# Kernel optimization log

Hardware: AMD Instinct MI355X
Metric: run time of the kernel (lower is better)

Reference implementation:

```python
import jax, jax.numpy as jnp
import numpy as np

B, S, D, H = 2, 2048, 1024, 16
DK = D // H


def setup_inputs() -> dict:
    key = jax.random.key(0)
    ks = jax.random.split(key, 9)
    s = 1.0 / np.sqrt(D)
    return {
        "x": jax.random.normal(ks[0], (B, S, D), dtype=jnp.float32),
        "wq": jax.random.normal(ks[1], (D, D), dtype=jnp.float32) * s,
        "bq": jax.random.normal(ks[2], (D,), dtype=jnp.float32) * 0.01,
        "wk": jax.random.normal(ks[3], (D, D), dtype=jnp.float32) * s,
        "bk": jax.random.normal(ks[4], (D,), dtype=jnp.float32) * 0.01,
        "wv": jax.random.normal(ks[5], (D, D), dtype=jnp.float32) * s,
        "bv": jax.random.normal(ks[6], (D,), dtype=jnp.float32) * 0.01,
        "wo": jax.random.normal(ks[7], (D, D), dtype=jnp.float32) * s,
        "bo": jax.random.normal(ks[8], (D,), dtype=jnp.float32) * 0.01,
    }


def reference(x, wq, bq, wk, bk, wv, bv, wo, bo):
    b, s, d = x.shape
    # Linear layers use torch convention: y = x @ W.T + b
    def proj(w, bias):
        y = jnp.einsum("bsd,ed->bse", x, w) + bias
        return y.reshape(b, s, H, DK).transpose(0, 2, 1, 3)  # (B,H,S,DK)

    q = proj(wq, bq)
    k = proj(wk, bk)
    v = proj(wv, bv)

    # Because each Q-chunk attends to the full K/V with m initialized to -inf,
    # the chunked online-softmax loop is exactly full softmax attention.
    scores = jnp.einsum("bhqd,bhkd->bhqk", q, k) / jnp.sqrt(jnp.float32(DK))
    attn = jax.nn.softmax(scores, axis=-1)
    out = jnp.einsum("bhqk,bhkd->bhqd", attn, v)  # (B,H,S,DK)

    out = out.transpose(0, 2, 1, 3).reshape(b, s, d)
    return jnp.einsum("bsd,ed->bse", out, wo) + bo
```

## Files before the change

kernel.cpp:

```cpp
#include <hip/hip_runtime.h>

typedef __attribute__((ext_vector_type(8))) short s16x8;
typedef __attribute__((ext_vector_type(4))) short s16x4;
typedef __attribute__((ext_vector_type(4))) float f32x4;

#define DEVI static __device__ __forceinline__

DEVI short f2bf(float f) {
  union { float f; unsigned u; } v; v.f = f;
  unsigned u = v.u;
  unsigned r = u + 0x7FFFu + ((u >> 16) & 1u);
  return (short)(r >> 16);
}
DEVI short f2bf_fast(float f) {
  union { float f; unsigned u; } v; v.f = f;
  return (short)((v.u + 0x8000u) >> 16);
}
DEVI float bf2f(short s) {
  union { unsigned u; float f; } v;
  v.u = ((unsigned)(unsigned short)s) << 16;
  return v.f;
}
DEVI f32x4 mfma16(s16x8 a, s16x8 b, f32x4 c) {
  return __builtin_amdgcn_mfma_f32_16x16x32_bf16(a, b, c, 0, 0, 0);
}
DEVI float fexp2(float x) {
#if __has_builtin(__builtin_amdgcn_exp2f)
  return __builtin_amdgcn_exp2f(x);
#else
  float r; asm("v_exp_f32 %0, %1" : "=v"(r) : "v"(x)); return r;
#endif
}
DEVI void gld16(const void* g, void* l) {
  __builtin_amdgcn_global_load_lds(
      (const __attribute__((address_space(1))) void*)g,
      (__attribute__((address_space(3))) void*)l, 16, 0, 0);
}

constexpr int Sc = 2048, Dc = 1024, Hc = 16, DKc = 64;
constexpr int Mc = 4096;

__global__ void detect_ker(const unsigned short* __restrict__ x, int* __restrict__ flag) {
  __shared__ int cnt;
  if (threadIdx.x == 0) cnt = 0;
  __syncthreads();
  int c = 0;
  for (int i = threadIdx.x; i < 4096; i += 256) {
    int e = (x[i] >> 7) & 0xFF;
    if (e >= 140) c++;
  }
  atomicAdd(&cnt, c);
  __syncthreads();
  if (threadIdx.x == 0) *flag = (cnt > 64) ? 1 : 0;
}

__global__ void norm_all(const void* x,
                         const void* w0, const void* w1, const void* w2, const void* w3,
                         const void* b0, const void* b1, const void* b2, const void* b3,
                         short* __restrict__ xdst, short* __restrict__ wdst,
                         float* __restrict__ bdst, const int* __restrict__ flag) {
  const int f = *flag;
  const int blk = blockIdx.x, tid = threadIdx.x;
  if (blk < 8192) {
    const void* src; short* dst; int i;
    if (blk < 4096) {
      i = blk * 256 + tid; src = x; dst = xdst;
    } else {
      int j = (blk - 4096) * 256 + tid;
      int region = j >> 18;
      const void* ws[4] = {w0, w1, w2, w3};
      src = ws[region]; dst = wdst + (size_t)region * 1048576;
      i = j & 262143;
    }
    if (f) {
      f32x4 v = ((const f32x4*)src)[i];
      s16x4 o;
#pragma unroll
      for (int j2 = 0; j2 < 4; ++j2) o[j2] = f2bf(v[j2]);
      ((s16x4*)dst)[i] = o;
    } else {
      ((s16x4*)dst)[i] = ((const s16x4*)src)[i];
    }
  } else {
    const void* bs[4] = {b0, b1, b2, b3};
#pragma unroll
    for (int j = 0; j < 16; ++j) {
      int i = tid + j * 256;
      int r = i >> 10, k = i & 1023;
      bdst[i] = f ? ((const float*)bs[r])[k] : bf2f(((const short*)bs[r])[k]);
    }
  }
}

template <int EPI>
__global__ __launch_bounds__(256, 2)
void gemm_bt(const short* __restrict__ A, const short* __restrict__ Wbase,
             const float* __restrict__ bias_c, short* __restrict__ outQKV,
             short* __restrict__ outV, void* __restrict__ outFinal,
             const int* __restrict__ flag) {
  constexpr int K = Dc, N = Dc;
  const int z = blockIdx.z;
  const short* W = Wbase + (size_t)z * N * K;
  const float* bias = bias_c + (size_t)z * N;
  const float oscale = (EPI == 0 && z == 0) ? 0.125f * 1.44269504f : 1.0f;

  __shared__ short lA[128 * 64];
  __shared__ short lB[128 * 64];

  const int tid = threadIdx.x;
  const int lane = tid & 63, wave = tid >> 6;
  const int l16 = lane & 15, quad = lane >> 4;
  const int wm0 = (wave >> 1) * 64, wn0 = (wave & 1) * 64;
  const int m0 = blockIdx.y * 128, n0 = blockIdx.x * 128;
  const int lr = lane >> 3;
  const int cg = ((lane & 7) ^ lr) * 8;
  const int x7 = l16 & 7;

  f32x4 acc[4][4] = {};

  for (int k0 = 0; k0 < K; k0 += 64) {
    __syncthreads();
#pragma unroll
    for (int it = 0; it < 4; ++it) {
      int rbase = wave * 32 + it * 8;
      gld16(&A[(size_t)(m0 + rbase + lr) * K + k0 + cg], &lA[rbase * 64]);
      gld16(&W[(size_t)(n0 + rbase + lr) * K + k0 + cg], &lB[rbase * 64]);
    }
    __syncthreads();
#pragma unroll
    for (int ks = 0; ks < 2; ++ks) {
      const int sw = ((ks * 4 + quad) ^ x7) * 8;
      s16x8 af[4], bfr[4];
#pragma unroll
      for (int i = 0; i < 4; ++i) {
        af[i]  = *(const s16x8*)&lA[(wm0 + i * 16 + l16) * 64 + sw];
        bfr[i] = *(const s16x8*)&lB[(wn0 + i * 16 + l16) * 64 + sw];
      }
#pragma unroll
      for (int mi = 0; mi < 4; ++mi)
#pragma unroll
        for (int ni = 0; ni < 4; ++ni)
          acc[mi][ni] = mfma16(af[mi], bfr[ni], acc[mi][ni]);
    }
  }

  if constexpr (EPI == 0) {
    if (z == 2) {
#pragma unroll
      for (int ni = 0; ni < 4; ++ni) {
        int n = n0 + wn0 + ni * 16 + l16;
        float bv = bias[n];
        int h = (n >> 6) & 15, dk = n & 63;
#pragma unroll
        for (int mi = 0; mi < 4; ++mi) {
          int mbase = m0 + wm0 + mi * 16 + quad * 4;
          int bb = mbase >> 11, s = mbase & 2047;
          s16x4 pk;
#pragma unroll
          for (int r = 0; r < 4; ++r) pk[r] = f2bf(acc[mi][ni][r] + bv);
          *(s16x4*)&outV[(((size_t)(bb * Hc + h)) * DKc + dk) * Sc + s] = pk;
        }
      }
      return;
    }
#pragma unroll
    for (int ni = 0; ni < 4; ++ni) {
      int n = n0 + wn0 + ni * 16 + l16;
      float bv = bias[n];
#pragma unroll
      for (int mi = 0; mi < 4; ++mi) {
#pragma unroll
        for (int r = 0; r < 4; ++r) {
          int m = m0 + wm0 + mi * 16 + quad * 4 + r;
          float v = (acc[mi][ni][r] + bv) * oscale;
          int bb = m >> 11, s = m & 2047, h = n >> 6, dk = n & 63;
          size_t idx = ((((size_t)bb * Hc + h) * Sc) + s) * DKc + dk +
                       (size_t)z * Mc * N;
          outQKV[idx] = f2bf(v);
        }
      }
    }
  } else {
    int f32out = *flag;
#pragma unroll
    for (int ni = 0; ni < 4; ++ni) {
      int n = n0 + wn0 + ni * 16 + l16;
      float bv = bias[n];
#pragma unroll
      for (int mi = 0; mi < 4; ++mi) {
#pragma unroll
        for (int r = 0; r < 4; ++r) {
          int m = m0 + wm0 + mi * 16 + quad * 4 + r;
          float v = acc[mi][ni][r] + bv;
          if (f32out) ((float*)outFinal)[(size_t)m * N + n] = v;
          else        ((short*)outFinal)[(size_t)m * N + n] = f2bf(v);
        }
      }
    }
  }
}

__global__ __launch_bounds__(256, 2)
void attn_ker(const short* __restrict__ Q, const short* __restrict__ Kg,
              const short* __restrict__ Vt, short* __restrict__ O) {
  __shared__ short lK[2][64 * 64];
  __shared__ short lV[2][64 * 64];
  __shared__ short lP[4][32][72];

  const int tid = threadIdx.x;
  const int lane = tid & 63, wave = tid >> 6;
  const int l16 = lane & 15, quad = lane >> 4;
  const int lr = lane >> 3;
  const int cg = ((lane & 7) ^ lr) * 8;
  const int x7 = l16 & 7;

  const int bh = blockIdx.y;
  const short* Qb = Q + (size_t)bh * Sc * DKc;
  const short* Kb = Kg + (size_t)bh * Sc * DKc;
  const short* Vb = Vt + (size_t)bh * DKc * Sc;

  const int q0 = blockIdx.x * 128 + wave * 32;

  s16x8 qf[2][2];
#pragma unroll
  for (int mi = 0; mi < 2; ++mi)
#pragma unroll
    for (int ks = 0; ks < 2; ++ks)
      qf[mi][ks] = *(const s16x8*)&Qb[(size_t)(q0 + mi * 16 + l16) * DKc + ks * 32 + quad * 8];

  s16x8 ones = {};
  if (l16 == 0) {
#pragma unroll
    for (int j = 0; j < 8; ++j) ones[j] = (short)0x3F80;
  }
  const f32x4 initC = {-24.f, -24.f, -24.f, -24.f};

  f32x4 oacc[2][4] = {};
  f32x4 oln[2] = {};

#define STAGE(BUF, KB)                                                          \
  {                                                                             \
    _Pragma("unroll")                                                           \
    for (int it = 0; it < 2; ++it) {                                            \
      int rbase = wave * 16 + it * 8;                                           \
      gld16(&Kb[(size_t)((KB) + rbase + lr) * DKc + cg], &lK[BUF][rbase * 64]); \
      gld16(&Vb[(size_t)(rbase + lr) * Sc + (KB) + cg], &lV[BUF][rbase * 64]);  \
    }                                                                           \
  }

  STAGE(0, 0)

  for (int kt = 0; kt < Sc / 64; ++kt) {
    const int p = kt & 1;
    __syncthreads();
    if (kt + 1 < Sc / 64) STAGE(p ^ 1, (kt + 1) * 64)

    f32x4 sacc[2][4];
    {
      const int sw0 = (quad ^ x7) * 8;
      s16x8 kf[4];
#pragma unroll
      for (int ni = 0; ni < 4; ++ni)
        kf[ni] = *(const s16x8*)&lK[p][(ni * 16 + l16) * 64 + sw0];
#pragma unroll
      for (int mi = 0; mi < 2; ++mi)
#pragma unroll
        for (int ni = 0; ni < 4; ++ni)
          sacc[mi][ni] = mfma16(qf[mi][0], kf[ni], initC);
    }
    {
      const int sw1 = ((4 + quad) ^ x7) * 8;
      s16x8 kf[4];
#pragma unroll
      for (int ni = 0; ni < 4; ++ni)
        kf[ni] = *(const s16x8*)&lK[p][(ni * 16 + l16) * 64 + sw1];
#pragma unroll
      for (int mi = 0; mi < 2; ++mi)
#pragma unroll
        for (int ni = 0; ni < 4; ++ni)
          sacc[mi][ni] = mfma16(qf[mi][1], kf[ni], sacc[mi][ni]);
    }

    s16x8 vf[2][4];
#pragma unroll
    for (int ks = 0; ks < 2; ++ks) {
      const int sw = ((ks * 4 + quad) ^ x7) * 8;
#pragma unroll
      for (int ni = 0; ni < 4; ++ni)
        vf[ks][ni] = *(const s16x8*)&lV[p][(ni * 16 + l16) * 64 + sw];
    }

#pragma unroll
    for (int mi = 0; mi < 2; ++mi)
#pragma unroll
      for (int r = 0; r < 4; ++r) {
        int row = mi * 16 + quad * 4 + r;
#pragma unroll
        for (int ni = 0; ni < 4; ++ni)
          lP[wave][row][ni * 16 + l16] = f2bf_fast(fexp2(sacc[mi][ni][r]));
      }

    __builtin_amdgcn_s_waitcnt(0xc07f);

    s16x8 pf[2][2];
#pragma unroll
    for (int mi = 0; mi < 2; ++mi)
#pragma unroll
      for (int ks = 0; ks < 2; ++ks)
        pf[mi][ks] = *(const s16x8*)&lP[wave][mi * 16 + l16][ks * 32 + quad * 8];

#pragma unroll
    for (int ks = 0; ks < 2; ++ks) {
#pragma unroll
      for (int mi = 0; mi < 2; ++mi) {
#pragma unroll
        for (int ni = 0; ni < 4; ++ni)
          oacc[mi][ni] = mfma16(pf[mi][ks], vf[ks][ni], oacc[mi][ni]);
        oln[mi] = mfma16(pf[mi][ks], ones, oln[mi]);
      }
    }
  }
#undef STAGE

  const int bb = bh >> 4, h = bh & 15;
#pragma unroll
  for (int mi = 0; mi < 2; ++mi) {
#pragma unroll
    for (int r = 0; r < 4; ++r) {
      float l = __shfl(oln[mi][r], lane & 48);
      float inv = 1.0f / l;
      int srow = q0 + mi * 16 + quad * 4 + r;
#pragma unroll
      for (int ni = 0; ni < 4; ++ni) {
        int col = h * DKc + ni * 16 + l16;
        O[((size_t)(bb * Sc + srow)) * Dc + col] = f2bf(oacc[mi][ni][r] * inv);
      }
    }
  }
}

extern "C" void kernel_launch(void* const* d_in, const int* in_sizes, int n_in,
                              void* d_out, int out_size, void* d_ws, size_t ws_size,
                              hipStream_t stream) {
  const void* x  = d_in[0];
  const void* wq = d_in[1]; const void* bq = d_in[2];
  const void* wk = d_in[3]; const void* bk = d_in[4];
  const void* wv = d_in[5]; const void* bv = d_in[6];
  const void* wo = d_in[7]; const void* bo = d_in[8];

  char* wsb = (char*)d_ws;
  int*   flag = (int*)wsb;
  short* x_c  = (short*)(wsb + 1024);
  short* w_c  = x_c + (size_t)4 * 1024 * 1024;
  float* b_c  = (float*)(wsb + 1024 + 16 * 1024 * 1024);
  short* Qc   = (short*)(wsb + 1024 + 16 * 1024 * 1024 + 16384);
  short* Kc   = Qc + (size_t)4 * 1024 * 1024;
  short* Vtc  = Kc + (size_t)4 * 1024 * 1024;
  short* Oc   = Vtc + (size_t)4 * 1024 * 1024;

  detect_ker<<<1, 256, 0, stream>>>((const unsigned short*)x, flag);

  norm_all<<<8193, 256, 0, stream>>>(x, wq, wk, wv, wo, bq, bk, bv, bo,
                                     x_c, w_c, b_c, flag);

  gemm_bt<0><<<dim3(8, 32, 3), 256, 0, stream>>>(x_c, w_c, b_c, Qc, Vtc,
                                                 nullptr, flag);

  attn_ker<<<dim3(16, 32), 256, 0, stream>>>(Qc, Kc, Vtc, Oc);

  gemm_bt<1><<<dim3(8, 32, 1), 256, 0, stream>>>(Oc, w_c + 3 * 1048576,
                                                 b_c + 3 * 1024, nullptr, nullptr,
                                                 d_out, flag);
}
```

Measured before the change: 214.4 us.

## Skip bf16 copy pass and split attention into 8 waves of 16 query rows

When the inputs are already bf16, the normalization kernel no longer copies x and the weights into the workspace. The GEMMs read the original buffers directly, picking them by the runtime flag. The attention kernel moves from 4 waves with 32 query rows each to 8 waves with 16 rows each at 512 threads. It also swaps grid axes so blocks sharing a head are adjacent, and computes P before loading V fragments. This cuts copy traffic and per-wave register pressure for more occupancy, at the cost of more K/V LDS reads per query row.

Result: faster. 204.8 us (-4.5%).

```diff
diff --git a/kernel.cpp b/kernel.cpp
--- a/kernel.cpp
+++ b/kernel.cpp
@@ -62,6 +62,7 @@
   const int f = *flag;
   const int blk = blockIdx.x, tid = threadIdx.x;
   if (blk < 8192) {
+    if (!f) return;
     const void* src; short* dst; int i;
     if (blk < 4096) {
       i = blk * 256 + tid; src = x; dst = xdst;
@@ -72,15 +73,11 @@
       src = ws[region]; dst = wdst + (size_t)region * 1048576;
       i = j & 262143;
     }
-    if (f) {
-      f32x4 v = ((const f32x4*)src)[i];
-      s16x4 o;
-#pragma unroll
-      for (int j2 = 0; j2 < 4; ++j2) o[j2] = f2bf(v[j2]);
-      ((s16x4*)dst)[i] = o;
-    } else {
-      ((s16x4*)dst)[i] = ((const s16x4*)src)[i];
-    }
+    f32x4 v = ((const f32x4*)src)[i];
+    s16x4 o;
+#pragma unroll
+    for (int j2 = 0; j2 < 4; ++j2) o[j2] = f2bf(v[j2]);
+    ((s16x4*)dst)[i] = o;
   } else {
     const void* bs[4] = {b0, b1, b2, b3};
 #pragma unroll
@@ -94,13 +91,18 @@
 
 template <int EPI>
 __global__ __launch_bounds__(256, 2)
-void gemm_bt(const short* __restrict__ A, const short* __restrict__ Wbase,
+void gemm_bt(const short* __restrict__ Aorig, const short* __restrict__ Acvt,
+             const short* __restrict__ W0, const short* __restrict__ W1,
+             const short* __restrict__ W2, const short* __restrict__ Wcvt,
              const float* __restrict__ bias_c, short* __restrict__ outQKV,
              short* __restrict__ outV, void* __restrict__ outFinal,
              const int* __restrict__ flag) {
   constexpr int K = Dc, N = Dc;
   const int z = blockIdx.z;
-  const short* W = Wbase + (size_t)z * N * K;
+  const int f = *flag;
+  const short* A = f ? Acvt : Aorig;
+  const short* Wor = (z == 0) ? W0 : (z == 1) ? W1 : W2;
+  const short* W = f ? (Wcvt + (size_t)z * 1048576) : Wor;
   const float* bias = bias_c + (size_t)z * N;
   const float oscale = (EPI == 0 && z == 0) ? 0.125f * 1.44269504f : 1.0f;
 
@@ -181,7 +183,6 @@
       }
     }
   } else {
-    int f32out = *flag;
 #pragma unroll
     for (int ni = 0; ni < 4; ++ni) {
       int n = n0 + wn0 + ni * 16 + l16;
@@ -192,20 +193,20 @@
         for (int r = 0; r < 4; ++r) {
           int m = m0 + wm0 + mi * 16 + quad * 4 + r;
           float v = acc[mi][ni][r] + bv;
-          if (f32out) ((float*)outFinal)[(size_t)m * N + n] = v;
-          else        ((short*)outFinal)[(size_t)m * N + n] = f2bf(v);
+          if (f) ((float*)outFinal)[(size_t)m * N + n] = v;
+          else   ((short*)outFinal)[(size_t)m * N + n] = f2bf(v);
         }
       }
     }
   }
 }
 
-__global__ __launch_bounds__(256, 2)
+__global__ __launch_bounds__(512, 4)
 void attn_ker(const short* __restrict__ Q, const short* __restrict__ Kg,
               const short* __restrict__ Vt, short* __restrict__ O) {
   __shared__ short lK[2][64 * 64];
   __shared__ short lV[2][64 * 64];
-  __shared__ short lP[4][32][72];
+  __shared__ short lP[8][16][72];
 
   const int tid = threadIdx.x;
   const int lane = tid & 63, wave = tid >> 6;
@@ -214,19 +215,17 @@
   const int cg = ((lane & 7) ^ lr) * 8;
   const int x7 = l16 & 7;
 
-  const int bh = blockIdx.y;
+  const int bh = blockIdx.x;
   const short* Qb = Q + (size_t)bh * Sc * DKc;
   const short* Kb = Kg + (size_t)bh * Sc * DKc;
   const short* Vb = Vt + (size_t)bh * DKc * Sc;
 
-  const int q0 = blockIdx.x * 128 + wave * 32;
-
-  s16x8 qf[2][2];
-#pragma unroll
-  for (int mi = 0; mi < 2; ++mi)
-#pragma unroll
-    for (int ks = 0; ks < 2; ++ks)
-      qf[mi][ks] = *(const s16x8*)&Qb[(size_t)(q0 + mi * 16 + l16) * DKc + ks * 32 + quad * 8];
+  const int q0 = blockIdx.y * 128 + wave * 16;
+
+  s16x8 qf[2];
+#pragma unroll
+  for (int ks = 0; ks < 2; ++ks)
+    qf[ks] = *(const s16x8*)&Qb[(size_t)(q0 + l16) * DKc + ks * 32 + quad * 8];
 
   s16x8 ones = {};
   if (l16 == 0) {
@@ -235,17 +234,14 @@
   }
   const f32x4 initC = {-24.f, -24.f, -24.f, -24.f};
 
-  f32x4 oacc[2][4] = {};
-  f32x4 oln[2] = {};
+  f32x4 oacc[4] = {};
+  f32x4 oln = {};
 
 #define STAGE(BUF, KB)                                                          \
   {                                                                             \
-    _Pragma("unroll")                                                           \
-    for (int it = 0; it < 2; ++it) {                                            \
-      int rbase = wave * 16 + it * 8;                                           \
-      gld16(&Kb[(size_t)((KB) + rbase + lr) * DKc + cg], &lK[BUF][rbase * 64]); \
-      gld16(&Vb[(size_t)(rbase + lr) * Sc + (KB) + cg], &lV[BUF][rbase * 64]);  \
-    }                                                                           \
+    int rbase = wave * 8;                                                       \
+    gld16(&Kb[(size_t)((KB) + rbase + lr) * DKc + cg], &lK[BUF][rbase * 64]);   \
+    gld16(&Vb[(size_t)(rbase + lr) * Sc + (KB) + cg], &lV[BUF][rbase * 64]);    \
   }
 
   STAGE(0, 0)
@@ -255,7 +251,7 @@
     __syncthreads();
     if (kt + 1 < Sc / 64) STAGE(p ^ 1, (kt + 1) * 64)
 
-    f32x4 sacc[2][4];
+    f32x4 sacc[4];
     {
       const int sw0 = (quad ^ x7) * 8;
       s16x8 kf[4];
@@ -263,10 +259,8 @@
       for (int ni = 0; ni < 4; ++ni)
         kf[ni] = *(const s16x8*)&lK[p][(ni * 16 + l16) * 64 + sw0];
 #pragma unroll
-      for (int mi = 0; mi < 2; ++mi)
-#pragma unroll
-        for (int ni = 0; ni < 4; ++ni)
-          sacc[mi][ni] = mfma16(qf[mi][0], kf[ni], initC);
+      for (int ni = 0; ni < 4; ++ni)
+        sacc[ni] = mfma16(qf[0], kf[ni], initC);
     }
     {
       const int sw1 = ((4 + quad) ^ x7) * 8;
@@ -275,10 +269,16 @@
       for (int ni = 0; ni < 4; ++ni)
         kf[ni] = *(const s16x8*)&lK[p][(ni * 16 + l16) * 64 + sw1];
 #pragma unroll
-      for (int mi = 0; mi < 2; ++mi)
-#pragma unroll
-        for (int ni = 0; ni < 4; ++ni)
-          sacc[mi][ni] = mfma16(qf[mi][1], kf[ni], sacc[mi][ni]);
+      for (int ni = 0; ni < 4; ++ni)
+        sacc[ni] = mfma16(qf[1], kf[ni], sacc[ni]);
+    }
+
+#pragma unroll
+    for (int r = 0; r < 4; ++r) {
+      int row = quad * 4 + r;
+#pragma unroll
+      for (int ni = 0; ni < 4; ++ni)
+        lP[wave][row][ni * 16 + l16] = f2bf_fast(fexp2(sacc[ni][r]));
     }
 
     s16x8 vf[2][4];
@@ -290,51 +290,33 @@
         vf[ks][ni] = *(const s16x8*)&lV[p][(ni * 16 + l16) * 64 + sw];
     }
 
-#pragma unroll
-    for (int mi = 0; mi < 2; ++mi)
-#pragma unroll
-      for (int r = 0; r < 4; ++r) {
-        int row = mi * 16 + quad * 4 + r;
-#pragma unroll
-        for (int ni = 0; ni < 4; ++ni)
-          lP[wave][row][ni * 16 + l16] = f2bf_fast(fexp2(sacc[mi][ni][r]));
-      }
-
     __builtin_amdgcn_s_waitcnt(0xc07f);
 
-    s16x8 pf[2][2];
-#pragma unroll
-    for (int mi = 0; mi < 2; ++mi)
-#pragma unroll
-      for (int ks = 0; ks < 2; ++ks)
-        pf[mi][ks] = *(const s16x8*)&lP[wave][mi * 16 + l16][ks * 32 + quad * 8];
+    s16x8 pf[2];
+#pragma unroll
+    for (int ks = 0; ks < 2; ++ks)
+      pf[ks] = *(const s16x8*)&lP[wave][l16][ks * 32 + quad * 8];
 
 #pragma unroll
     for (int ks = 0; ks < 2; ++ks) {
 #pragma unroll
-      for (int mi = 0; mi < 2; ++mi) {
-#pragma unroll
-        for (int ni = 0; ni < 4; ++ni)
-          oacc[mi][ni] = mfma16(pf[mi][ks], vf[ks][ni], oacc[mi][ni]);
-        oln[mi] = mfma16(pf[mi][ks], ones, oln[mi]);
-      }
+      for (int ni = 0; ni < 4; ++ni)
+        oacc[ni] = mfma16(pf[ks], vf[ks][ni], oacc[ni]);
+      oln = mfma16(pf[ks], ones, oln);
     }
   }
 #undef STAGE
 
   const int bb = bh >> 4, h = bh & 15;
 #pragma unroll
-  for (int mi = 0; mi < 2; ++mi) {
-#pragma unroll
-    for (int r = 0; r < 4; ++r) {
-      float l = __shfl(oln[mi][r], lane & 48);
-      float inv = 1.0f / l;
-      int srow = q0 + mi * 16 + quad * 4 + r;
-#pragma unroll
-      for (int ni = 0; ni < 4; ++ni) {
-        int col = h * DKc + ni * 16 + l16;
-        O[((size_t)(bb * Sc + srow)) * Dc + col] = f2bf(oacc[mi][ni][r] * inv);
-      }
+  for (int r = 0; r < 4; ++r) {
+    float l = __shfl(oln[r], lane & 48);
+    float inv = 1.0f / l;
+    int srow = q0 + quad * 4 + r;
+#pragma unroll
+    for (int ni = 0; ni < 4; ++ni) {
+      int col = h * DKc + ni * 16 + l16;
+      O[((size_t)(bb * Sc + srow)) * Dc + col] = f2bf(oacc[ni][r] * inv);
     }
   }
 }
@@ -363,12 +345,15 @@
   norm_all<<<8193, 256, 0, stream>>>(x, wq, wk, wv, wo, bq, bk, bv, bo,
                                      x_c, w_c, b_c, flag);
 
-  gemm_bt<0><<<dim3(8, 32, 3), 256, 0, stream>>>(x_c, w_c, b_c, Qc, Vtc,
-                                                 nullptr, flag);
-
-  attn_ker<<<dim3(16, 32), 256, 0, stream>>>(Qc, Kc, Vtc, Oc);
-
-  gemm_bt<1><<<dim3(8, 32, 1), 256, 0, stream>>>(Oc, w_c + 3 * 1048576,
-                                                 b_c + 3 * 1024, nullptr, nullptr,
-                                                 d_out, flag);
-}
+  gemm_bt<0><<<dim3(8, 32, 3), 256, 0, stream>>>(
+      (const short*)x, x_c,
+      (const short*)wq, (const short*)wk, (const short*)wv, w_c,
+      b_c, Qc, Vtc, nullptr, flag);
+
+  attn_ker<<<dim3(32, 16), 512, 0, stream>>>(Qc, Kc, Vtc, Oc);
+
+  gemm_bt<1><<<dim3(8, 32, 1), 256, 0, stream>>>(
+      Oc, Oc,
+      (const short*)wo, (const short*)wo, (const short*)wo, w_c + 3 * 1048576,
+      b_c + 3 * 1024, nullptr, nullptr, d_out, flag);
+}
```
